# Kernel optimization log

Measured on AMD Instinct MI355X. Metric: run time of the kernel, lower is better.

## Reference

```python
import jax, jax.numpy as jnp
import numpy as np

P = np.pi
PARENTS = np.array([0,0,0,0,1,2,3,4,5,6,7,8,9,9,9,12,13,14,16,17,18,19,20,21])
VERTS_LIST = np.array([1325,336,1032,4515,1374,4848,1739,5209,1960,5423])
SYNTH = np.array([3,15,4,5,7,8,18,19,20,21])

def _bounds():
    b = [[-0.5933865286111969,0.5933865286111969],[-2*P,2*P],[-1.215762200416361,1.215762200416361],
         [-1.5793940868065197,0.3097956806],[-0.5881754611,0.5689768556],[-0.5323249722,0.6736965222],
         [-1.5793940868065197,0.3097956806],[-0.5689768556,0.5881754611],[-0.6736965222,0.5323249722],
         [-P/3,P/3],[-P/36,P/36],[-P/36,P/36],
         [-0.02268926111,2.441713561],[-0.01,0.01],[-0.01,0.01],
         [-0.02268926111,2.441713561],[-0.01,0.01],[-0.01,0.01],
         [-P/3,P/3],[-P/36,P/36],[-P/36,P/36]]
    b += [[-P/6,P/6]]*6
    b += [[-P/3,P/3],[-P/36,P/36],[-P/36,P/36]]
    b += [[-0.01,0.01]]*6
    b += [[-P/3,P/3],[-P/36,P/36],[-P/36,P/36]]
    k = [(-1.551596394,2.206094311),(-2.455676183,0.7627082389),(-1.570795,2.188641033),
         (-1.551596394,2.206094311),(-0.7627082389,2.455676183),(-2.188641033,1.570795)]
    b += [[a/3.0,c/3.0] for a,c in k]
    b += [[-P/3,P/3],[-P/36,P/36],[-P/36,P/36]]
    b += [[a*2.0/3.0,c*2.0/3.0] for a,c in k]
    b += [[-0.01,0.01],[-2.570867817,0.04799651389],[-0.01,0.01],[-0.01,0.01],[-0.04799651389,2.570867817],[-0.01,0.01]]
    b += [[-P/6,P/6]]*6
    b += [[-0.01,0.01]]*6
    return 2.0*jnp.asarray(np.array(b, np.float32))  # [72,2]

def quat2mat(q):
    q = q / jnp.linalg.norm(q, axis=1, keepdims=True)
    w, x, y, z = q[:,0], q[:,1], q[:,2], q[:,3]
    r0 = jnp.stack([1-2*(y*y+z*z), 2*(x*y-w*z), 2*(x*z+w*y)], -1)
    r1 = jnp.stack([2*(x*y+w*z), 1-2*(x*x+z*z), 2*(y*z-w*x)], -1)
    r2 = jnp.stack([2*(x*z-w*y), 2*(y*z+w*x), 1-2*(x*x+y*y)], -1)
    return jnp.stack([r0, r1, r2], 1)

def batch_rodrigues(theta):  # [N,3] axis-angle -> [N,3,3]
    angle = jnp.linalg.norm(theta + 1e-8, axis=1, keepdims=True)
    half = angle * 0.5
    q = jnp.concatenate([jnp.cos(half), (theta/angle)*jnp.sin(half)], axis=1)
    return quat2mat(q)

def global_rigid_transform(Rs, Js):  # Rs [B,24,3,3], Js [B,24,3]
    B = Rs.shape[0]
    dt = Rs.dtype
    def make_A(R, t):
        Rh = jnp.concatenate([R, jnp.zeros((B,1,3), dt)], axis=1)       # [B,4,3]
        th = jnp.concatenate([t, jnp.ones((B,1), dt)], axis=1)[:,:,None] # [B,4,1]
        return jnp.concatenate([Rh, th], axis=2)                          # [B,4,4]
    results = [make_A(Rs[:,0], Js[:,0])]
    for i in range(1, 24):  # fixed 24-joint kinematic chain
        p = int(PARENTS[i])
        results.append(results[p] @ make_A(Rs[:,i], Js[:,i]-Js[:,p]))
    G = jnp.stack(results, axis=1)  # [B,24,4,4]
    new_J = G[:,:,:3,3]
    Jh = jnp.concatenate([Js, jnp.zeros((B,24,1), dt)], axis=2)[...,None]
    init_bone = jnp.pad(G @ Jh, ((0,0),(0,0),(0,0),(3,0)))
    return new_J, G - init_bone

def setup_inputs():
    key = jax.random.key(0)
    ks = jax.random.split(key, 7)
    B, R = 256, 6890
    x = jax.random.normal(ks[0], (B, 88), jnp.float32)
    g = jax.nn.one_hot(jax.random.randint(ks[1], (B,), 0, 2), 2, dtype=jnp.float32)
    v_template = jax.random.normal(ks[2], (2, R, 3), jnp.float32) * 0.3
    shapedirs = jax.random.normal(ks[3], (2, 10, R, 3), jnp.float32) * 0.01
    Jr = jax.random.uniform(ks[4], (2, R, 24), jnp.float32) ** 8
    J_regressor = Jr / Jr.sum(axis=1, keepdims=True)
    posedirs = jax.random.normal(ks[5], (2, R, 3, 207), jnp.float32) * 0.01
    w = jax.random.uniform(ks[6], (2, R, 24), jnp.float32) ** 8
    weights = w / w.sum(axis=2, keepdims=True)
    return {"x": x, "batch_gender": g, "v_template": v_template, "shapedirs": shapedirs,
            "J_regressor": J_regressor, "posedirs": posedirs, "weights": weights}

def reference(x, batch_gender, v_template, shapedirs, J_regressor, posedirs, weights):
    B = x.shape[0]
    bounds = _bounds()
    # is_gt=False path: root-shift offsets, then pad 88->91 with the atan2 root angles spliced in
    x = x.at[:,10].add(0.6-0.286).at[:,11].add(1.2-0.286).at[:,12].add(0.1)
    betas = jnp.tanh(x[:, :10] / 3.0) * 3.0
    root_shift = x[:, 10:13]
    root_angles = x[:, 13:19]
    root_rot = jnp.stack([jnp.arctan2(x[:,16], x[:,13]),
                          jnp.arctan2(x[:,17], x[:,14]),
                          jnp.arctan2(x[:,18], x[:,15])], axis=1)
    pose = jnp.concatenate([root_rot, x[:, 19:88]], axis=1)  # [B,72]
    mean_b = bounds.mean(axis=1)
    scale = 2.0 / jnp.abs(bounds[:,0] - bounds[:,1])
    pose = jnp.tanh((pose - mean_b) * scale) / scale + mean_b
    Rs = batch_rodrigues(pose.reshape(-1, 3)).reshape(B, 24, 3, 3)
    g = batch_gender  # [B,2]
    vt = jnp.einsum('bg,grd->brd', g, v_template)
    bsm = jnp.einsum('bk,gkrd->gbrd', betas, shapedirs)  # per-gender shape blendshapes
    v_shaped = jnp.einsum('bg,gbrd->brd', g, bsm) + vt   # [B,R,3]
    Jg = jnp.einsum('brd,grj->bgjd', v_shaped, J_regressor)
    J = jnp.einsum('bg,bgjd->bjd', g, Jg)  # [B,24,3]
    new_J, A = global_rigid_transform(Rs, J)
    new_J = new_J - J[:, 0:1] + root_shift[:, None, :]
    pose_feat = (Rs[:, 1:] - jnp.eye(3, dtype=Rs.dtype)).reshape(B, 207)
    pcon = jnp.einsum('bp,grdp->gbrd', pose_feat, posedirs)  # per-gender pose blendshapes
    v_posed = jnp.einsum('bg,gbrd->brd', g, pcon) + v_shaped
    w = jnp.einsum('bg,grj->brj', g, weights)             # [B,R,24]
    T = jnp.einsum('brj,bjpq->brpq', w, A)                # [B,R,4,4]
    verts = jnp.einsum('brij,brj->bri', T[:,:,:3,:3], v_posed) + T[:,:,:3,3]
    verts = verts - J[:, 0:1] + root_shift[:, None, :]
    verts_red = verts[:, VERTS_LIST, :]
    verts_offset = jax.lax.stop_gradient(verts_red) - jax.lax.stop_gradient(new_J[:, SYNTH, :])
    return betas, pose, root_shift, root_angles, verts, verts_red, new_J, verts_offset
```

## Files before the change

### kernel.cpp

```cpp
#include <hip/hip_runtime.h>
#include <hip/hip_bf16.h>


#define NB 256
#define NR 6890
#define NJ 24
#define RD3 (NR*3)
#define KPD 207
#define K2C 8
#define K2R 862
#define NT4 431
#define BROW 232
#define VROWB 264

#define OFF_BETAS 0
#define OFF_POSE  2560
#define OFF_RSH   20992
#define OFF_RA    21760
#define OFF_VERTS 23296
#define OFF_VRED  5314816
#define OFF_NEWJ  5322496
#define OFF_VOFF  5340928

#define WS_RS    0
#define WS_PF    55296
#define WS_BETA  108288
#define WS_RSH   110848
#define WS_GI    111616
#define WS_ORD   111872
#define WS_CNT   112128
#define WS_PFB   112904
#define WS_AT    170248

typedef short v8s __attribute__((ext_vector_type(8)));
typedef float v4f __attribute__((ext_vector_type(4)));

__constant__ int PAR_c[24] = {0,0,0,0,1,2,3,4,5,6,7,8,9,9,9,12,13,14,16,17,18,19,20,21};
__constant__ int VL_c[10]  = {1325,336,1032,4515,1374,4848,1739,5209,1960,5423};
__constant__ int SY_c[10]  = {3,15,4,5,7,8,18,19,20,21};
__constant__ int LVL_j[23]  = {1,2,3, 4,5,6, 7,8,9, 10,11,12,13,14, 15,16,17, 18,19, 20,21, 22,23};
__constant__ int LVL_off[9] = {0,3,6,9,14,17,19,21,23};

__constant__ float BLO[72] = {
  -0.5933865286111969f, -6.283185307179586f, -1.215762200416361f,
  -1.5793940868065197f, -0.5881754611f, -0.5323249722f,
  -1.5793940868065197f, -0.5689768556f, -0.6736965222f,
  -1.0471975511965976f, -0.08726646259971647f, -0.08726646259971647f,
  -0.02268926111f, -0.01f, -0.01f,
  -0.02268926111f, -0.01f, -0.01f,
  -1.0471975511965976f, -0.08726646259971647f, -0.08726646259971647f,
  -0.5235987755982988f, -0.5235987755982988f, -0.5235987755982988f,
  -0.5235987755982988f, -0.5235987755982988f, -0.5235987755982988f,
  -1.0471975511965976f, -0.08726646259971647f, -0.08726646259971647f,
  -0.01f, -0.01f, -0.01f, -0.01f, -0.01f, -0.01f,
  -1.0471975511965976f, -0.08726646259971647f, -0.08726646259971647f,
  (float)(-1.551596394/3.0), (float)(-2.455676183/3.0), (float)(-1.570795/3.0),
  (float)(-1.551596394/3.0), (float)(-0.7627082389/3.0), (float)(-2.188641033/3.0),
  -1.0471975511965976f, -0.08726646259971647f, -0.08726646259971647f,
  (float)(-1.551596394*2.0/3.0), (float)(-2.455676183*2.0/3.0), (float)(-1.570795*2.0/3.0),
  (float)(-1.551596394*2.0/3.0), (float)(-0.7627082389*2.0/3.0), (float)(-2.188641033*2.0/3.0),
  -0.01f, -2.570867817f, -0.01f, -0.01f, -0.04799651389f, -0.01f,
  -0.5235987755982988f, -0.5235987755982988f, -0.5235987755982988f,
  -0.5235987755982988f, -0.5235987755982988f, -0.5235987755982988f,
  -0.01f, -0.01f, -0.01f, -0.01f, -0.01f, -0.01f
};
__constant__ float BHI[72] = {
  0.5933865286111969f, 6.283185307179586f, 1.215762200416361f,
  0.3097956806f, 0.5689768556f, 0.6736965222f,
  0.3097956806f, 0.5881754611f, 0.5323249722f,
  1.0471975511965976f, 0.08726646259971647f, 0.08726646259971647f,
  2.441713561f, 0.01f, 0.01f,
  2.441713561f, 0.01f, 0.01f,
  1.0471975511965976f, 0.08726646259971647f, 0.08726646259971647f,
  0.5235987755982988f, 0.5235987755982988f, 0.5235987755982988f,
  0.5235987755982988f, 0.5235987755982988f, 0.5235987755982988f,
  1.0471975511965976f, 0.08726646259971647f, 0.08726646259971647f,
  0.01f, 0.01f, 0.01f, 0.01f, 0.01f, 0.01f,
  1.0471975511965976f, 0.08726646259971647f, 0.08726646259971647f,
  (float)(2.206094311/3.0), (float)(0.7627082389/3.0), (float)(2.188641033/3.0),
  (float)(2.206094311/3.0), (float)(2.455676183/3.0), (float)(1.570795/3.0),
  1.0471975511965976f, 0.08726646259971647f, 0.08726646259971647f,
  (float)(2.206094311*2.0/3.0), (float)(0.7627082389*2.0/3.0), (float)(2.188641033*2.0/3.0),
  (float)(2.206094311*2.0/3.0), (float)(2.455676183*2.0/3.0), (float)(1.570795*2.0/3.0),
  0.01f, 0.04799651389f, 0.01f, 0.01f, 2.570867817f, 0.01f,
  0.5235987755982988f, 0.5235987755982988f, 0.5235987755982988f,
  0.5235987755982988f, 0.5235987755982988f, 0.5235987755982988f,
  0.01f, 0.01f, 0.01f, 0.01f, 0.01f, 0.01f
};

__device__ __forceinline__ unsigned short f2bf(float f) {
  union { float f; unsigned u; } c; c.f = f;
  const unsigned u = c.u + 0x7FFFu + ((c.u >> 16) & 1u);
  return (unsigned short)(u >> 16);
}
__device__ __forceinline__ float bf2f(unsigned short h) {
  union { unsigned u; float f; } c; c.u = (unsigned)h << 16; return c.f;
}

__global__ void kA_front(const float* __restrict__ x, const float* __restrict__ gen,
                         const float* __restrict__ vtemp, const float* __restrict__ sdirs,
                         const float* __restrict__ jreg,
                         float* __restrict__ out, float* __restrict__ W)
{
  const int bid = blockIdx.x;
  const int tid = threadIdx.x;

  if (bid < NB) {
    const int b = bid;
    const float* xb = x + b * 88;
    if (tid < 24) {
      const int j = tid;
      float t[3];
      if (j == 0) {
        t[0] = atan2f(xb[16], xb[13]);
        t[1] = atan2f(xb[17], xb[14]);
        t[2] = atan2f(xb[18], xb[15]);
      } else {
        t[0] = xb[19 + (j - 1) * 3 + 0];
        t[1] = xb[19 + (j - 1) * 3 + 1];
        t[2] = xb[19 + (j - 1) * 3 + 2];
      }
#pragma unroll
      for (int c = 0; c < 3; c++) {
        const int pi = j * 3 + c;
        const float lo = 2.f * BLO[pi], hi = 2.f * BHI[pi];
        const float mean = 0.5f * (lo + hi);
        const float scale = 2.f / fabsf(lo - hi);
        const float v = tanhf((t[c] - mean) * scale) / scale + mean;
        t[c] = v;
        out[OFF_POSE + b * 72 + pi] = v;
      }
      const float a0 = t[0] + 1e-8f, a1 = t[1] + 1e-8f, a2 = t[2] + 1e-8f;
      const float ang = sqrtf(a0 * a0 + a1 * a1 + a2 * a2);
      const float half = 0.5f * ang;
      const float sh = sinf(half), ch = cosf(half);
      const float inv = sh / ang;
      float qw = ch, qx = t[0] * inv, qy = t[1] * inv, qz = t[2] * inv;
      const float nn = sqrtf(qw * qw + qx * qx + qy * qy + qz * qz);
      qw /= nn; qx /= nn; qy /= nn; qz /= nn;
      float R[9];
      R[0] = 1.f - 2.f * (qy * qy + qz * qz); R[1] = 2.f * (qx * qy - qw * qz); R[2] = 2.f * (qx * qz + qw * qy);
      R[3] = 2.f * (qx * qy + qw * qz); R[4] = 1.f - 2.f * (qx * qx + qz * qz); R[5] = 2.f * (qy * qz - qw * qx);
      R[6] = 2.f * (qx * qz - qw * qy); R[7] = 2.f * (qy * qz + qw * qx); R[8] = 1.f - 2.f * (qx * qx + qy * qy);
      float* rsw = W + WS_RS + (size_t)(b * 24 + j) * 9;
#pragma unroll
      for (int e = 0; e < 9; e++) rsw[e] = R[e];
      if (j >= 1) {
        float* pfw = W + WS_PF + (size_t)b * 207 + (j - 1) * 9;
#pragma unroll
        for (int e = 0; e < 9; e++)
          pfw[e] = R[e] - ((e == 0 || e == 4 || e == 8) ? 1.f : 0.f);
      }
    } else if (tid < 34) {
      const int k = tid - 24;
      const float v = tanhf(xb[k] / 3.0f) * 3.0f;
      out[OFF_BETAS + b * 10 + k] = v;
      W[WS_BETA + b * 10 + k] = v;
    } else if (tid == 34) {
      const float r0 = xb[10] + (0.6f - 0.286f);
      const float r1 = xb[11] + (1.2f - 0.286f);
      const float r2 = xb[12] + 0.1f;
      out[OFF_RSH + b * 3 + 0] = r0; out[OFF_RSH + b * 3 + 1] = r1; out[OFF_RSH + b * 3 + 2] = r2;
      W[WS_RSH + b * 3 + 0] = r0; W[WS_RSH + b * 3 + 1] = r1; W[WS_RSH + b * 3 + 2] = r2;
#pragma unroll
      for (int k2 = 0; k2 < 6; k2++) out[OFF_RA + b * 6 + k2] = xb[13 + k2];
    } else if (tid == 35) {
      ((int*)(W + WS_GI))[b] = (gen[b * 2 + 1] > gen[b * 2 + 0]) ? 1 : 0;
    }
    return;
  }

  const int kb = bid - NB;
  const int c = kb % K2C, j = (kb / K2C) % 24, g = kb / (K2C * 24);
  const int r0 = c * K2R;
  int r1 = r0 + K2R; if (r1 > NR) r1 = NR;
  const float* vtg = vtemp + (size_t)g * NR * 3;
  const float* sdg = sdirs + (size_t)g * 10 * NR * 3;
  const float* jrg = jreg + (size_t)g * NR * 24;
  float acc[33];
#pragma unroll
  for (int e = 0; e < 33; e++) acc[e] = 0.f;
  for (int r = r0 + tid; r < r1; r += 256) {
    const float w = jrg[r * 24 + j];
    acc[0] += vtg[r * 3 + 0] * w;
    acc[1] += vtg[r * 3 + 1] * w;
    acc[2] += vtg[r * 3 + 2] * w;
#pragma unroll
    for (int k = 0; k < 10; k++) {
      const float* s = sdg + ((size_t)k * NR + r) * 3;
      acc[3 + k * 3 + 0] += s[0] * w;
      acc[3 + k * 3 + 1] += s[1] * w;
      acc[3 + k * 3 + 2] += s[2] * w;
    }
  }
  __shared__ float red[4][33];
  const int lane = tid & 63, wv = tid >> 6;
#pragma unroll
  for (int e = 0; e < 33; e++) {
    float v = acc[e];
    v += __shfl_down(v, 32); v += __shfl_down(v, 16); v += __shfl_down(v, 8);
    v += __shfl_down(v, 4);  v += __shfl_down(v, 2);  v += __shfl_down(v, 1);
    if (lane == 0) red[wv][e] = v;
  }
  __syncthreads();
  if (tid < 33) {
    const int e = tid;
    out[OFF_VERTS + (size_t)(((g * 24 + j) * K2C + c) * 33 + e)] =
        red[0][e] + red[1][e] + red[2][e] + red[3][e];
  }
}

__global__ void kB_mid(float* __restrict__ out, float* __restrict__ W)
{
  const int bid = blockIdx.x;
  const int tid = threadIdx.x;

  if (bid < 512) {
    __shared__ int s_ord[NB];
    __shared__ int s_c0[4];
    const int gib = ((const int*)(W + WS_GI))[tid];
    const int lane = tid & 63, wvi = tid >> 6;
    const unsigned long long b0 = __ballot(gib == 0);
    if (lane == 0) s_c0[wvi] = __popcll(b0);
    __syncthreads();
    const int t0 = s_c0[0] + s_c0[1] + s_c0[2] + s_c0[3];
    int off0 = 0, off1 = t0;
    for (int w = 0; w < wvi; w++) { off0 += s_c0[w]; off1 += 64 - s_c0[w]; }
    const unsigned long long ltm = (1ull << lane) - 1ull;
    const int rr0 = __popcll(b0 & ltm);
    const int rr1 = lane - rr0;
    if (gib == 0) s_ord[off0 + rr0] = tid;
    else          s_ord[off1 + rr1] = tid;
    __syncthreads();

    if (bid == 0) {
      ((int*)(W + WS_ORD))[tid] = s_ord[tid];
      if (tid == 0) { ((int*)(W + WS_CNT))[0] = t0; ((int*)(W + WS_CNT))[1] = NB - t0; }
    }

    const int g = bid >> 8, m = bid & 255;
    const int n_g = g ? (NB - t0) : t0;
    const int g0off = g ? t0 : 0;
    if (tid < 224) {
      float v = 0.f;
      if (m < n_g) {
        const int b = s_ord[g0off + m];
        if (tid < KPD)        v = W[WS_PF + (size_t)b * KPD + tid];
        else if (tid < 217)   v = W[WS_BETA + b * 10 + (tid - KPD)];
        else if (tid == 217)  v = 1.f;
      }
      ((unsigned short*)(W + WS_PFB))[((size_t)g * 256 + m) * 224 + tid] = f2bf(v);
    }
    return;
  }

  const int b = bid - 512;
  __shared__ float J[72];
  __shared__ float G[24][12];
  __shared__ float sA[24][12];
  __shared__ float j0s[3];
  const int gi = ((const int*)(W + WS_GI))[b];
  float bb[10];
#pragma unroll
  for (int k = 0; k < 10; k++) bb[k] = W[WS_BETA + b * 10 + k];

  if (tid < 72) {
    const int j = tid / 3, d = tid % 3;
    float v = 0.f;
#pragma unroll
    for (int c = 0; c < K2C; c++) {
      const float* P = out + OFF_VERTS + (size_t)(((gi * 24 + j) * K2C + c) * 33);
      float s = P[d];
#pragma unroll
      for (int k = 0; k < 10; k++) s += bb[k] * P[3 + k * 3 + d];
      v += s;
    }
    J[tid] = v;
  }
  __syncthreads();
  const float* Rs = W + WS_RS + (size_t)b * 216;
  if (tid < 12) {
    const int row = tid / 4, col = tid % 4;
    G[0][tid] = (col < 3) ? Rs[row * 3 + col] : J[row];
  }
  __syncthreads();
#pragma unroll
  for (int L = 0; L < 8; L++) {
    const int base = LVL_off[L];
    const int cntL = LVL_off[L + 1] - base;
    const int slot = tid / 12, e = tid - slot * 12;
    if (slot < cntL) {
      const int i = LVL_j[base + slot];
      const int p = PAR_c[i];
      const int row = e / 4, col = e - row * 4;
      const float* Ri = Rs + i * 9;
      const float g0 = G[p][row * 4 + 0], g1 = G[p][row * 4 + 1], g2 = G[p][row * 4 + 2];
      float v;
      if (col < 3) {
        v = g0 * Ri[col] + g1 * Ri[3 + col] + g2 * Ri[6 + col];
      } else {
        const float t0 = J[i * 3 + 0] - J[p * 3 + 0];
        const float t1 = J[i * 3 + 1] - J[p * 3 + 1];
        const float t2 = J[i * 3 + 2] - J[p * 3 + 2];
        v = g0 * t0 + g1 * t1 + g2 * t2 + G[p][row * 4 + 3];
      }
      G[i][e] = v;
    }
    __syncthreads();
  }
  if (tid < 3)
    j0s[tid] = W[WS_RSH + b * 3 + tid] - J[tid];
  __syncthreads();
  if (tid < 72) {
    const int j = tid / 3, d = tid % 3;
    out[OFF_NEWJ + (size_t)b * 72 + tid] = G[j][d * 4 + 3] + j0s[d];
  }
  for (int e = tid; e < 288; e += 256) {
    const int j = e / 12, rc = e - j * 12, row = rc / 4, col = rc - row * 4;
    float v = G[j][rc];
    if (col == 3)
      v -= G[j][row * 4 + 0] * J[j * 3 + 0] + G[j][row * 4 + 1] * J[j * 3 + 1] + G[j][row * 4 + 2] * J[j * 3 + 2];
    sA[j][rc] = v;
  }
  __syncthreads();
  unsigned short* at = (unsigned short*)(W + WS_AT) + (size_t)b * 768;
  for (int e = tid; e < 384; e += 256) {
    const int c = e >> 5, j = e & 31;
    float a = 0.f;
    if (j < 24) a = sA[j][c];
    else if (j == 24) a = ((c & 3) == 3) ? j0s[c >> 2] : 0.f;
    const unsigned short h = f2bf(a);
    const unsigned short l = f2bf(a - bf2f(h));
    at[c * 32 + j] = h;
    at[384 + c * 32 + j] = l;
  }
}

__launch_bounds__(512, 2)
__global__ void k4_fused(const float* __restrict__ pd, const float* __restrict__ vtemp,
                         const float* __restrict__ sdirs, const float* __restrict__ wts,
                         float* __restrict__ out, const float* __restrict__ W)
{
  __shared__ __align__(16) unsigned short bsm[48][BROW];
  __shared__ __align__(16) unsigned short vps[48][VROWB];
  __shared__ int s_ord[NB];

  const int tid = threadIdx.x;
  const int wave = tid >> 6, lane = tid & 63;
  const int g = blockIdx.y;
  const int nfrac = lane & 15;
  const int kq = (lane >> 4) * 8;
  const int tile = blockIdx.x;
  const int n0 = tile * 48;
  const int rbase = tile * 16;

  const int* cnt = (const int*)(W + WS_CNT);
  const int* ord = (const int*)(W + WS_ORD);
  const int nh = cnt[g];
  const int g0off = g ? cnt[0] : 0;
  if (nh <= 0) return;

  if (tid < NB) s_ord[tid] = ord[tid];

  const int nrows = (RD3 - n0 < 48) ? (RD3 - n0) : 48;
  const int nflat = nrows * KPD;
  const float* src = pd + ((size_t)g * RD3 + n0) * KPD;
#pragma unroll
  for (int i = 0; i < 5; i++) {
    const int e4 = (i * 512 + tid) * 4;
    if (e4 + 3 < nflat) {
      float t4[4];
      __builtin_memcpy(t4, src + e4, 16);
#pragma unroll
      for (int t = 0; t < 4; t++) {
        const int fl = e4 + t;
        bsm[fl / KPD][fl % KPD] = f2bf(t4[t]);
      }
    } else if (e4 < nflat) {
      for (int t = 0; t < 4 && e4 + t < nflat; t++)
        bsm[(e4 + t) / KPD][(e4 + t) % KPD] = f2bf(src[e4 + t]);
    }
  }
  if (tid < 480) {
    const int r_ = tid / 10, kk = tid - r_ * 10;
    const int nr = (n0 + r_ < RD3) ? (n0 + r_) : (RD3 - 1);
    const int rr = nr / 3, dd = nr - rr * 3;
    bsm[r_][KPD + kk] = f2bf(sdirs[((size_t)(g * 10 + kk) * NR + rr) * 3 + dd]);
  }
  if (tid >= 464) {
    const int r_ = tid - 464;
    const int nr = (n0 + r_ < RD3) ? (n0 + r_) : (RD3 - 1);
    const int rr = nr / 3, dd = nr - rr * 3;
    bsm[r_][217] = f2bf(vtemp[((size_t)g * NR + rr) * 3 + dd]);
  }
  if (tid < 288) {
    const int r_ = tid / 6, kk = 218 + (tid - r_ * 6);
    bsm[r_][kk] = 0;
  }
  __syncthreads();

  const unsigned short* pfb = (const unsigned short*)(W + WS_PFB) + (size_t)g * 256 * 224;
  const int mtmax = (nh + 15) >> 4;
  for (int mt = wave; mt < mtmax; mt += 8) {
    const unsigned short* ap = pfb + (size_t)(mt * 16 + nfrac) * 224 + kq;
    v8s af[7];
#pragma unroll
    for (int c = 0; c < 7; c++) af[c] = *(const v8s*)(ap + c * 32);
#pragma unroll
    for (int s = 0; s < 3; s++) {
      const unsigned short* bp = &bsm[s * 16 + nfrac][0];
      v8s bfr[7];
#pragma unroll
      for (int c = 0; c < 7; c++) bfr[c] = *(const v8s*)(bp + c * 32 + kq);

      v4f acc0 = {0.f, 0.f, 0.f, 0.f};
      v4f acc1 = {0.f, 0.f, 0.f, 0.f};
      acc0 = __builtin_amdgcn_mfma_f32_16x16x32_bf16(af[0], bfr[0], acc0, 0, 0, 0);
      acc1 = __builtin_amdgcn_mfma_f32_16x16x32_bf16(af[1], bfr[1], acc1, 0, 0, 0);
      acc0 = __builtin_amdgcn_mfma_f32_16x16x32_bf16(af[2], bfr[2], acc0, 0, 0, 0);
      acc1 = __builtin_amdgcn_mfma_f32_16x16x32_bf16(af[3], bfr[3], acc1, 0, 0, 0);
      acc0 = __builtin_amdgcn_mfma_f32_16x16x32_bf16(af[4], bfr[4], acc0, 0, 0, 0);
      acc1 = __builtin_amdgcn_mfma_f32_16x16x32_bf16(af[5], bfr[5], acc1, 0, 0, 0);
      acc0 = __builtin_amdgcn_mfma_f32_16x16x32_bf16(af[6], bfr[6], acc0, 0, 0, 0);

      const int ln = s * 16 + nfrac;
      const int lm0 = mt * 16 + (lane >> 4) * 4;
#pragma unroll
      for (int j = 0; j < 4; j++)
        vps[ln][lm0 + j] = f2bf(acc0[j] + acc1[j]);
    }
  }
  __syncthreads();

  const int f = nfrac, q = lane >> 4;
  const int r = rbase + f;
  const int rc = (r < NR) ? r : (NR - 1);

  int vli = -1;
#pragma unroll
  for (int i = 0; i < 10; i++) if (r == VL_c[i]) vli = i;
  const int syj = (vli >= 0) ? SY_c[vli] : 0;

  v8s wh, wl;
  {
    union { v8s v; unsigned short s[8]; } H, L;
    if (q < 3) {
      float fw[8];
      __builtin_memcpy(fw, wts + ((size_t)g * NR + rc) * 24 + q * 8, 32);
#pragma unroll
      for (int t = 0; t < 8; t++) { H.s[t] = f2bf(fw[t]); L.s[t] = f2bf(fw[t] - bf2f(H.s[t])); }
    } else {
#pragma unroll
      for (int t = 0; t < 8; t++) { H.s[t] = (t == 0) ? 0x3F80 : 0; L.s[t] = 0; }
    }
    wh = H.v; wl = L.v;
  }

  const unsigned short* at = (const unsigned short*)(W + WS_AT);
  const int fragoff = f * 32 + q * 8;

  for (int lm = wave; lm < nh; lm += 16) {
    const int lmB = lm + 8;
    const bool hasB = (lmB < nh);
    const int lmBc = hasB ? lmB : lm;
    const int b1 = s_ord[g0off + lm];
    const int b2 = s_ord[g0off + lmBc];
    const v8s ah1 = *(const v8s*)(at + (size_t)b1 * 768 + fragoff);
    const v8s al1 = *(const v8s*)(at + (size_t)b1 * 768 + 384 + fragoff);
    const v8s ah2 = *(const v8s*)(at + (size_t)b2 * 768 + fragoff);
    const v8s al2 = *(const v8s*)(at + (size_t)b2 * 768 + 384 + fragoff);
    const float vx1 = bf2f(vps[f * 3 + 0][lm]);
    const float vy1 = bf2f(vps[f * 3 + 1][lm]);
    const float vz1 = bf2f(vps[f * 3 + 2][lm]);
    const float vx2 = bf2f(vps[f * 3 + 0][lmBc]);
    const float vy2 = bf2f(vps[f * 3 + 1][lmBc]);
    const float vz2 = bf2f(vps[f * 3 + 2][lmBc]);

    v4f accA = {0.f, 0.f, 0.f, 0.f};
    v4f accB = {0.f, 0.f, 0.f, 0.f};
    accA = __builtin_amdgcn_mfma_f32_16x16x32_bf16(ah1, wh, accA, 0, 0, 0);
    accB = __builtin_amdgcn_mfma_f32_16x16x32_bf16(ah2, wh, accB, 0, 0, 0);
    accA = __builtin_amdgcn_mfma_f32_16x16x32_bf16(ah1, wl, accA, 0, 0, 0);
    accB = __builtin_amdgcn_mfma_f32_16x16x32_bf16(ah2, wl, accB, 0, 0, 0);
    accA = __builtin_amdgcn_mfma_f32_16x16x32_bf16(al1, wh, accA, 0, 0, 0);
    accB = __builtin_amdgcn_mfma_f32_16x16x32_bf16(al2, wh, accB, 0, 0, 0);

    const float o1 = accA[0] * vx1 + accA[1] * vy1 + accA[2] * vz1 + accA[3];
    const float o2 = accB[0] * vx2 + accB[1] * vy2 + accB[2] * vz2 + accB[3];
    if (q < 3 && r < NR) {
      out[OFF_VERTS + ((size_t)b1 * NR + r) * 3 + q] = o1;
      if (hasB) out[OFF_VERTS + ((size_t)b2 * NR + r) * 3 + q] = o2;
      if (vli >= 0) {
        out[OFF_VRED + ((size_t)b1 * 10 + vli) * 3 + q] = o1;
        out[OFF_VOFF + ((size_t)b1 * 10 + vli) * 3 + q] =
            o1 - out[OFF_NEWJ + (size_t)b1 * 72 + syj * 3 + q];
        if (hasB) {
          out[OFF_VRED + ((size_t)b2 * 10 + vli) * 3 + q] = o2;
          out[OFF_VOFF + ((size_t)b2 * 10 + vli) * 3 + q] =
              o2 - out[OFF_NEWJ + (size_t)b2 * 72 + syj * 3 + q];
        }
      }
    }
  }
}

extern "C" void kernel_launch(void* const* d_in, const int* in_sizes, int n_in,
                              void* d_out, int out_size, void* d_ws, size_t ws_size,
                              hipStream_t stream)
{
  const float* x   = (const float*)d_in[0];
  const float* gen = (const float*)d_in[1];
  const float* vt  = (const float*)d_in[2];
  const float* sd  = (const float*)d_in[3];
  const float* jr  = (const float*)d_in[4];
  const float* pd  = (const float*)d_in[5];
  const float* wt  = (const float*)d_in[6];
  float* out = (float*)d_out;
  float* W   = (float*)d_ws;

  kA_front<<<NB + 2 * 24 * K2C, 256, 0, stream>>>(x, gen, vt, sd, jr, out, W);
  kB_mid<<<512 + NB, 256, 0, stream>>>(out, W);
  k4_fused<<<dim3(NT4, 2), 512, 0, stream>>>(pd, vt, sd, wt, out, W);
}
```

Baseline: 68.47 us.

## Halve vps LDS buffer, process batch in 128-wide chunks, raise occupancy

The posed-vertex LDS buffer shrinks to 128 batch columns, and the blend-GEMM plus skinning phases now alternate per 128-sample chunk, with barriers between them. LDS per block drops, and the launch bound is raised from 2 to 8 blocks per CU to allow more concurrent blocks. The posedirs staging is rewritten as per-wave row loads with the shapedir and template fill merged into one loop. The extra barriers and the tighter register cap may add stalls or spills.

```diff
diff --git a/kernel.cpp b/kernel.cpp
--- a/kernel.cpp
+++ b/kernel.cpp
@@ -11,7 +11,7 @@
 #define K2R 862
 #define NT4 431
 #define BROW 232
-#define VROWB 264
+#define VROWB 132
 
 #define OFF_BETAS 0
 #define OFF_POSE  2560
@@ -336,7 +336,7 @@
   }
 }
 
-__launch_bounds__(512, 2)
+__launch_bounds__(512, 8)
 __global__ void k4_fused(const float* __restrict__ pd, const float* __restrict__ vtemp,
                          const float* __restrict__ sdirs, const float* __restrict__ wts,
                          float* __restrict__ out, const float* __restrict__ W)
@@ -362,80 +362,39 @@
 
   if (tid < NB) s_ord[tid] = ord[tid];
 
-  const int nrows = (RD3 - n0 < 48) ? (RD3 - n0) : 48;
-  const int nflat = nrows * KPD;
-  const float* src = pd + ((size_t)g * RD3 + n0) * KPD;
-#pragma unroll
-  for (int i = 0; i < 5; i++) {
-    const int e4 = (i * 512 + tid) * 4;
-    if (e4 + 3 < nflat) {
-      float t4[4];
-      __builtin_memcpy(t4, src + e4, 16);
-#pragma unroll
-      for (int t = 0; t < 4; t++) {
-        const int fl = e4 + t;
-        bsm[fl / KPD][fl % KPD] = f2bf(t4[t]);
-      }
-    } else if (e4 < nflat) {
-      for (int t = 0; t < 4 && e4 + t < nflat; t++)
-        bsm[(e4 + t) / KPD][(e4 + t) % KPD] = f2bf(src[e4 + t]);
-    }
-  }
-  if (tid < 480) {
-    const int r_ = tid / 10, kk = tid - r_ * 10;
+  {
+    const int row0 = wave * 6;
+#pragma unroll
+    for (int rr_ = 0; rr_ < 6; rr_++) {
+      const int row = row0 + rr_;
+      const int nr = (n0 + row < RD3) ? (n0 + row) : (RD3 - 1);
+      const float* rp = pd + ((size_t)g * RD3 + nr) * KPD;
+      const float c0 = rp[lane];
+      const float c1 = rp[lane + 64];
+      const float c2 = rp[lane + 128];
+      const float c3 = (lane + 192 < KPD) ? rp[lane + 192] : 0.f;
+      bsm[row][lane]       = f2bf(c0);
+      bsm[row][lane + 64]  = f2bf(c1);
+      bsm[row][lane + 128] = f2bf(c2);
+      const int c3col = lane + 192;
+      if (c3col < KPD)                      bsm[row][c3col] = f2bf(c3);
+      else if (c3col >= 218 && c3col < 224) bsm[row][c3col] = 0;
+    }
+  }
+  for (int e = tid; e < 528; e += 512) {
+    const int r_ = e / 11, kk = e - r_ * 11;
     const int nr = (n0 + r_ < RD3) ? (n0 + r_) : (RD3 - 1);
-    const int rr = nr / 3, dd = nr - rr * 3;
-    bsm[r_][KPD + kk] = f2bf(sdirs[((size_t)(g * 10 + kk) * NR + rr) * 3 + dd]);
-  }
-  if (tid >= 464) {
-    const int r_ = tid - 464;
-    const int nr = (n0 + r_ < RD3) ? (n0 + r_) : (RD3 - 1);
-    const int rr = nr / 3, dd = nr - rr * 3;
-    bsm[r_][217] = f2bf(vtemp[((size_t)g * NR + rr) * 3 + dd]);
-  }
-  if (tid < 288) {
-    const int r_ = tid / 6, kk = 218 + (tid - r_ * 6);
-    bsm[r_][kk] = 0;
-  }
-  __syncthreads();
-
-  const unsigned short* pfb = (const unsigned short*)(W + WS_PFB) + (size_t)g * 256 * 224;
-  const int mtmax = (nh + 15) >> 4;
-  for (int mt = wave; mt < mtmax; mt += 8) {
-    const unsigned short* ap = pfb + (size_t)(mt * 16 + nfrac) * 224 + kq;
-    v8s af[7];
-#pragma unroll
-    for (int c = 0; c < 7; c++) af[c] = *(const v8s*)(ap + c * 32);
-#pragma unroll
-    for (int s = 0; s < 3; s++) {
-      const unsigned short* bp = &bsm[s * 16 + nfrac][0];
-      v8s bfr[7];
-#pragma unroll
-      for (int c = 0; c < 7; c++) bfr[c] = *(const v8s*)(bp + c * 32 + kq);
-
-      v4f acc0 = {0.f, 0.f, 0.f, 0.f};
-      v4f acc1 = {0.f, 0.f, 0.f, 0.f};
-      acc0 = __builtin_amdgcn_mfma_f32_16x16x32_bf16(af[0], bfr[0], acc0, 0, 0, 0);
-      acc1 = __builtin_amdgcn_mfma_f32_16x16x32_bf16(af[1], bfr[1], acc1, 0, 0, 0);
-      acc0 = __builtin_amdgcn_mfma_f32_16x16x32_bf16(af[2], bfr[2], acc0, 0, 0, 0);
-      acc1 = __builtin_amdgcn_mfma_f32_16x16x32_bf16(af[3], bfr[3], acc1, 0, 0, 0);
-      acc0 = __builtin_amdgcn_mfma_f32_16x16x32_bf16(af[4], bfr[4], acc0, 0, 0, 0);
-      acc1 = __builtin_amdgcn_mfma_f32_16x16x32_bf16(af[5], bfr[5], acc1, 0, 0, 0);
-      acc0 = __builtin_amdgcn_mfma_f32_16x16x32_bf16(af[6], bfr[6], acc0, 0, 0, 0);
-
-      const int ln = s * 16 + nfrac;
-      const int lm0 = mt * 16 + (lane >> 4) * 4;
-#pragma unroll
-      for (int j = 0; j < 4; j++)
-        vps[ln][lm0 + j] = f2bf(acc0[j] + acc1[j]);
-    }
+    const int rrr = nr / 3, dd = nr - rrr * 3;
+    if (kk < 10)
+      bsm[r_][KPD + kk] = f2bf(sdirs[((size_t)(g * 10 + kk) * NR + rrr) * 3 + dd]);
+    else
+      bsm[r_][217] = f2bf(vtemp[((size_t)g * NR + rrr) * 3 + dd]);
   }
   __syncthreads();
 
   const int f = nfrac, q = lane >> 4;
   const int r = rbase + f;
   const int rc = (r < NR) ? r : (NR - 1);
-
   int vli = -1;
 #pragma unroll
   for (int i = 0; i < 10; i++) if (r == VL_c[i]) vli = i;
@@ -456,51 +415,92 @@
     wh = H.v; wl = L.v;
   }
 
+  const unsigned short* pfb = (const unsigned short*)(W + WS_PFB) + (size_t)g * 256 * 224;
   const unsigned short* at = (const unsigned short*)(W + WS_AT);
   const int fragoff = f * 32 + q * 8;
-
-  for (int lm = wave; lm < nh; lm += 16) {
-    const int lmB = lm + 8;
-    const bool hasB = (lmB < nh);
-    const int lmBc = hasB ? lmB : lm;
-    const int b1 = s_ord[g0off + lm];
-    const int b2 = s_ord[g0off + lmBc];
-    const v8s ah1 = *(const v8s*)(at + (size_t)b1 * 768 + fragoff);
-    const v8s al1 = *(const v8s*)(at + (size_t)b1 * 768 + 384 + fragoff);
-    const v8s ah2 = *(const v8s*)(at + (size_t)b2 * 768 + fragoff);
-    const v8s al2 = *(const v8s*)(at + (size_t)b2 * 768 + 384 + fragoff);
-    const float vx1 = bf2f(vps[f * 3 + 0][lm]);
-    const float vy1 = bf2f(vps[f * 3 + 1][lm]);
-    const float vz1 = bf2f(vps[f * 3 + 2][lm]);
-    const float vx2 = bf2f(vps[f * 3 + 0][lmBc]);
-    const float vy2 = bf2f(vps[f * 3 + 1][lmBc]);
-    const float vz2 = bf2f(vps[f * 3 + 2][lmBc]);
-
-    v4f accA = {0.f, 0.f, 0.f, 0.f};
-    v4f accB = {0.f, 0.f, 0.f, 0.f};
-    accA = __builtin_amdgcn_mfma_f32_16x16x32_bf16(ah1, wh, accA, 0, 0, 0);
-    accB = __builtin_amdgcn_mfma_f32_16x16x32_bf16(ah2, wh, accB, 0, 0, 0);
-    accA = __builtin_amdgcn_mfma_f32_16x16x32_bf16(ah1, wl, accA, 0, 0, 0);
-    accB = __builtin_amdgcn_mfma_f32_16x16x32_bf16(ah2, wl, accB, 0, 0, 0);
-    accA = __builtin_amdgcn_mfma_f32_16x16x32_bf16(al1, wh, accA, 0, 0, 0);
-    accB = __builtin_amdgcn_mfma_f32_16x16x32_bf16(al2, wh, accB, 0, 0, 0);
-
-    const float o1 = accA[0] * vx1 + accA[1] * vy1 + accA[2] * vz1 + accA[3];
-    const float o2 = accB[0] * vx2 + accB[1] * vy2 + accB[2] * vz2 + accB[3];
-    if (q < 3 && r < NR) {
-      out[OFF_VERTS + ((size_t)b1 * NR + r) * 3 + q] = o1;
-      if (hasB) out[OFF_VERTS + ((size_t)b2 * NR + r) * 3 + q] = o2;
-      if (vli >= 0) {
-        out[OFF_VRED + ((size_t)b1 * 10 + vli) * 3 + q] = o1;
-        out[OFF_VOFF + ((size_t)b1 * 10 + vli) * 3 + q] =
-            o1 - out[OFF_NEWJ + (size_t)b1 * 72 + syj * 3 + q];
-        if (hasB) {
-          out[OFF_VRED + ((size_t)b2 * 10 + vli) * 3 + q] = o2;
-          out[OFF_VOFF + ((size_t)b2 * 10 + vli) * 3 + q] =
-              o2 - out[OFF_NEWJ + (size_t)b2 * 72 + syj * 3 + q];
+  const int mtmax = (nh + 15) >> 4;
+
+  for (int half = 0; half * 128 < nh; half++) {
+    const int mtlo = half * 8;
+    const int mthi = (mtmax < mtlo + 8) ? mtmax : (mtlo + 8);
+
+    for (int mt = mtlo + wave; mt < mthi; mt += 8) {
+      const unsigned short* ap = pfb + (size_t)(mt * 16 + nfrac) * 224 + kq;
+      v8s af[7];
+#pragma unroll
+      for (int c = 0; c < 7; c++) af[c] = *(const v8s*)(ap + c * 32);
+#pragma unroll
+      for (int s = 0; s < 3; s++) {
+        const unsigned short* bp = &bsm[s * 16 + nfrac][0];
+        v8s bfr[7];
+#pragma unroll
+        for (int c = 0; c < 7; c++) bfr[c] = *(const v8s*)(bp + c * 32 + kq);
+
+        v4f acc0 = {0.f, 0.f, 0.f, 0.f};
+        v4f acc1 = {0.f, 0.f, 0.f, 0.f};
+        acc0 = __builtin_amdgcn_mfma_f32_16x16x32_bf16(af[0], bfr[0], acc0, 0, 0, 0);
+        acc1 = __builtin_amdgcn_mfma_f32_16x16x32_bf16(af[1], bfr[1], acc1, 0, 0, 0);
+        acc0 = __builtin_amdgcn_mfma_f32_16x16x32_bf16(af[2], bfr[2], acc0, 0, 0, 0);
+        acc1 = __builtin_amdgcn_mfma_f32_16x16x32_bf16(af[3], bfr[3], acc1, 0, 0, 0);
+        acc0 = __builtin_amdgcn_mfma_f32_16x16x32_bf16(af[4], bfr[4], acc0, 0, 0, 0);
+        acc1 = __builtin_amdgcn_mfma_f32_16x16x32_bf16(af[5], bfr[5], acc1, 0, 0, 0);
+        acc0 = __builtin_amdgcn_mfma_f32_16x16x32_bf16(af[6], bfr[6], acc0, 0, 0, 0);
+
+        const int ln = s * 16 + nfrac;
+        const int lm0 = (mt - mtlo) * 16 + (lane >> 4) * 4;
+#pragma unroll
+        for (int j = 0; j < 4; j++)
+          vps[ln][lm0 + j] = f2bf(acc0[j] + acc1[j]);
+      }
+    }
+    __syncthreads();
+
+    const int lmlo = half * 128;
+    const int lmhi = (nh < lmlo + 128) ? nh : (lmlo + 128);
+    for (int lm = lmlo + wave; lm < lmhi; lm += 16) {
+      const int lmB = lm + 8;
+      const bool hasB = (lmB < lmhi);
+      const int lmBc = hasB ? lmB : lm;
+      const int b1 = s_ord[g0off + lm];
+      const int b2 = s_ord[g0off + lmBc];
+      const v8s ah1 = *(const v8s*)(at + (size_t)b1 * 768 + fragoff);
+      const v8s al1 = *(const v8s*)(at + (size_t)b1 * 768 + 384 + fragoff);
+      const v8s ah2 = *(const v8s*)(at + (size_t)b2 * 768 + fragoff);
+      const v8s al2 = *(const v8s*)(at + (size_t)b2 * 768 + 384 + fragoff);
+      const float vx1 = bf2f(vps[f * 3 + 0][lm - lmlo]);
+      const float vy1 = bf2f(vps[f * 3 + 1][lm - lmlo]);
+      const float vz1 = bf2f(vps[f * 3 + 2][lm - lmlo]);
+      const float vx2 = bf2f(vps[f * 3 + 0][lmBc - lmlo]);
+      const float vy2 = bf2f(vps[f * 3 + 1][lmBc - lmlo]);
+      const float vz2 = bf2f(vps[f * 3 + 2][lmBc - lmlo]);
+
+      v4f accA = {0.f, 0.f, 0.f, 0.f};
+      v4f accB = {0.f, 0.f, 0.f, 0.f};
+      accA = __builtin_amdgcn_mfma_f32_16x16x32_bf16(ah1, wh, accA, 0, 0, 0);
+      accB = __builtin_amdgcn_mfma_f32_16x16x32_bf16(ah2, wh, accB, 0, 0, 0);
+      accA = __builtin_amdgcn_mfma_f32_16x16x32_bf16(ah1, wl, accA, 0, 0, 0);
+      accB = __builtin_amdgcn_mfma_f32_16x16x32_bf16(ah2, wl, accB, 0, 0, 0);
+      accA = __builtin_amdgcn_mfma_f32_16x16x32_bf16(al1, wh, accA, 0, 0, 0);
+      accB = __builtin_amdgcn_mfma_f32_16x16x32_bf16(al2, wh, accB, 0, 0, 0);
+
+      const float o1 = accA[0] * vx1 + accA[1] * vy1 + accA[2] * vz1 + accA[3];
+      const float o2 = accB[0] * vx2 + accB[1] * vy2 + accB[2] * vz2 + accB[3];
+      if (q < 3 && r < NR) {
+        out[OFF_VERTS + ((size_t)b1 * NR + r) * 3 + q] = o1;
+        if (hasB) out[OFF_VERTS + ((size_t)b2 * NR + r) * 3 + q] = o2;
+        if (vli >= 0) {
+          out[OFF_VRED + ((size_t)b1 * 10 + vli) * 3 + q] = o1;
+          out[OFF_VOFF + ((size_t)b1 * 10 + vli) * 3 + q] =
+              o1 - out[OFF_NEWJ + (size_t)b1 * 72 + syj * 3 + q];
+          if (hasB) {
+            out[OFF_VRED + ((size_t)b2 * 10 + vli) * 3 + q] = o2;
+            out[OFF_VOFF + ((size_t)b2 * 10 + vli) * 3 + q] =
+                o2 - out[OFF_NEWJ + (size_t)b2 * 72 + syj * 3 + q];
+          }
         }
       }
     }
+    __syncthreads();
   }
 }
 
```

Result: slower. 111.5 us (+62.8%).
